# Kernel optimization log

Hardware: AMD Instinct MI355X
Metric: run time of the kernel (lower is better)

The kernel has to match this reference:

```python
import jax, jax.numpy as jnp
import numpy as np

B, T, D = 128, 32, 1024
ADA, INTER, RANK = 1024, 1024, 8
LN_EPS = 1e-5

def setup_inputs() -> dict:
    key = jax.random.key(0)
    ks = jax.random.split(key, 9)
    return {
        "x": jax.random.normal(ks[0], (B, T, D), dtype=jnp.float32),
        "ada_emb": jax.random.normal(ks[1], (B, ADA), dtype=jnp.float32),
        "base_layer": jax.random.normal(ks[2], (D, D), dtype=jnp.float32),  # torch.randn init
        "w1": jax.random.normal(ks[3], (ADA, INTER), dtype=jnp.float32) * 0.02,
        "b1": jnp.zeros((INTER,), dtype=jnp.float32),
        "w2": jax.random.normal(ks[4], (INTER, 2 * D * RANK), dtype=jnp.float32) * 0.02,
        "b2": jnp.zeros((2 * D * RANK,), dtype=jnp.float32),
        "ln_g": jnp.ones((ADA,), dtype=jnp.float32),
        "ln_b": jnp.zeros((ADA,), dtype=jnp.float32),
    }

def _layernorm(x, g, b):
    mu = jnp.mean(x, axis=-1, keepdims=True)
    var = jnp.var(x, axis=-1, keepdims=True)
    return (x - mu) * jax.lax.rsqrt(var + LN_EPS) * g + b

def reference(x, ada_emb, base_layer, w1, b1, w2, b2, ln_g, ln_b):
    b, t, d = x.shape
    # hypernetwork: cond -> per-sample LoRA factors
    ae = _layernorm(ada_emb, ln_g, ln_b)
    h = jax.nn.gelu(ae @ w1 + b1, approximate=False)  # nn.GELU is exact (erf)
    xw = h @ w2 + b2                                   # (B, 2*D*rank)
    x_a, x_b = jnp.split(xw, 2, axis=-1)
    x_a = x_a.reshape(b, d, RANK)
    x_b = x_b.reshape(b, d, RANK)
    # fused per-sample weight: base + x_a @ x_b^T  -> (B, D, D)
    layer = base_layer[None, :, :] + jnp.einsum('bdr,bkr->bdk', x_a, x_b)
    # apply shared per-sample weight to every token (equiv to repeat_interleave + bmm)
    out = jnp.einsum('btc,bco->bto', x, layer)
    return x + out  # residual=True
```

## Files before the change

kernel.cpp:

```cpp
#include <hip/hip_runtime.h>
#include <hip/hip_bf16.h>
#include <math.h>

#define BB    128
#define TT    32
#define DD    1024
#define NADA  1024
#define NINT  1024
#define NRANK 8
#define LNEPS 1e-5f
#define SPL2  8
#define XWN   (2 * DD * NRANK)

using bf16x8 = __attribute__((ext_vector_type(8))) short;
using f32x4  = __attribute__((ext_vector_type(4))) float;

__device__ __forceinline__ short f2bf(float f) {
    __hip_bfloat16 h = __float2bfloat16(f);
    return *reinterpret_cast<short*>(&h);
}

__device__ __forceinline__ void async16(const void* g, void* l) {
    __builtin_amdgcn_global_load_lds(
        (const __attribute__((address_space(1))) void*)g,
        (__attribute__((address_space(3))) void*)l, 16, 0, 0);
}

__device__ __forceinline__ void tcast_tile(
    const float* __restrict__ in, short* __restrict__ out, int K, int N,
    int bx, int by, bool addI, int tid, float (*t)[68])
{
    const int n0 = bx * 64, k0 = by * 64;
    #pragma unroll
    for (int it = 0; it < 4; ++it) {
        const int idx = it * 256 + tid;
        const int r = idx >> 4, c4 = (idx & 15) * 4;
        float4 v = *(const float4*)(in + (size_t)(k0 + r) * N + n0 + c4);
        t[r][c4 + 0] = v.x; t[r][c4 + 1] = v.y;
        t[r][c4 + 2] = v.z; t[r][c4 + 3] = v.w;
    }
    __syncthreads();
    #pragma unroll
    for (int it = 0; it < 4; ++it) {
        const int idx = it * 256 + tid;
        const int rn = idx >> 4, c4 = (idx & 15) * 4;
        float f0 = t[c4 + 0][rn], f1 = t[c4 + 1][rn];
        float f2 = t[c4 + 2][rn], f3 = t[c4 + 3][rn];
        if (addI) {
            const int n = n0 + rn;
            if (k0 + c4 + 0 == n) f0 += 1.f;
            if (k0 + c4 + 1 == n) f1 += 1.f;
            if (k0 + c4 + 2 == n) f2 += 1.f;
            if (k0 + c4 + 3 == n) f3 += 1.f;
        }
        short4 p;
        p.x = f2bf(f0); p.y = f2bf(f1); p.z = f2bf(f2); p.w = f2bf(f3);
        *(short4*)(out + (size_t)(n0 + rn) * K + k0 + c4) = p;
    }
}

__global__ __launch_bounds__(256) void prep_kernel(
    const float* __restrict__ x, const float* __restrict__ w1,
    const float* __restrict__ base, const float* __restrict__ ada,
    const float* __restrict__ lng, const float* __restrict__ lnb,
    short* __restrict__ x_bf, short* __restrict__ w1t,
    short* __restrict__ baset, short* __restrict__ ae_bf)
{
    __shared__ float t[64][68];
    const int bid = blockIdx.x, tid = threadIdx.x;

    if (bid < 2048) {
        const int i0 = bid * 512 + tid;
        float4 v0 = reinterpret_cast<const float4*>(x)[i0];
        float4 v1 = reinterpret_cast<const float4*>(x)[i0 + 256];
        short4 p0, p1;
        p0.x = f2bf(v0.x); p0.y = f2bf(v0.y); p0.z = f2bf(v0.z); p0.w = f2bf(v0.w);
        p1.x = f2bf(v1.x); p1.y = f2bf(v1.y); p1.z = f2bf(v1.z); p1.w = f2bf(v1.w);
        reinterpret_cast<short4*>(x_bf)[i0] = p0;
        reinterpret_cast<short4*>(x_bf)[i0 + 256] = p1;
    } else if (bid < 2304) {
        const int b = bid - 2048;
        tcast_tile(w1, w1t, NADA, NINT, b & 15, b >> 4, false, tid, t);
    } else if (bid < 2560) {
        const int b = bid - 2304;
        tcast_tile(base, baset, DD, DD, b & 15, b >> 4, true, tid, t);
    } else {
        const int b = bid - 2560;
        const float* row = ada + (size_t)b * NADA;
        float sum = 0.f, sumsq = 0.f;
        for (int i = tid; i < NADA; i += 256) {
            float v = row[i];
            sum += v; sumsq += v * v;
        }
        #pragma unroll
        for (int off = 32; off > 0; off >>= 1) {
            sum   += __shfl_down(sum, off);
            sumsq += __shfl_down(sumsq, off);
        }
        float* s1 = &t[0][0];
        float* s2 = &t[1][0];
        const int wid = tid >> 6, lane = tid & 63;
        if (lane == 0) { s1[wid] = sum; s2[wid] = sumsq; }
        __syncthreads();
        if (tid == 0) {
            float a = 0.f, c = 0.f;
            for (int i = 0; i < 4; ++i) { a += s1[i]; c += s2[i]; }
            s1[0] = a; s2[0] = c;
        }
        __syncthreads();
        const float mu  = s1[0] * (1.f / NADA);
        const float var = s2[0] * (1.f / NADA) - mu * mu;
        const float inv = rsqrtf(var + LNEPS);
        for (int i = tid; i < NADA; i += 256) {
            ae_bf[(size_t)b * NADA + i] = f2bf((row[i] - mu) * inv * lng[i] + lnb[i]);
        }
    }
}

__global__ __launch_bounds__(256, 2) void mgemm2(
    const short* __restrict__ A, const short* __restrict__ Bt,
    float* __restrict__ C, int kLen)
{
    constexpr int BM = 64, BN = 64;
    __shared__ __align__(16) short As[BM * 64];
    __shared__ __align__(16) short Bs[BN * 64];

    const int bm = blockIdx.y * BM;
    const int bn = blockIdx.x * BN;
    const int kStart = blockIdx.z * kLen;
    const int tid = threadIdx.x;
    const int wave = tid >> 6, lane = tid & 63;
    const int wm0 = (wave >> 1) * 32;
    const int wn0 = (wave & 1) * 32;
    const int quad = lane >> 4, r16 = lane & 15;

    f32x4 acc[2][2] = {};

    for (int kt = 0; kt < kLen; kt += 64) {
        const int k0 = kStart + kt;
        #pragma unroll
        for (int kk = 0; kk < 2; ++kk) {
            async16(A + (size_t)(bm + (tid >> 2)) * NADA + k0 + kk * 32 + (tid & 3) * 8,
                    &As[kk * 2048 + tid * 8]);
            async16(Bt + (size_t)(bn + (tid >> 2)) * NADA + k0 + kk * 32 + (tid & 3) * 8,
                    &Bs[kk * 2048 + tid * 8]);
        }
        __syncthreads();
        #pragma unroll
        for (int kk = 0; kk < 2; ++kk) {
            bf16x8 af[2], bfr[2];
            #pragma unroll
            for (int i = 0; i < 2; ++i)
                af[i] = *reinterpret_cast<const bf16x8*>(
                    &As[kk * 2048 + (wm0 + i * 16 + r16) * 32 + quad * 8]);
            #pragma unroll
            for (int j = 0; j < 2; ++j)
                bfr[j] = *reinterpret_cast<const bf16x8*>(
                    &Bs[kk * 2048 + (wn0 + j * 16 + r16) * 32 + quad * 8]);
            #pragma unroll
            for (int i = 0; i < 2; ++i)
                #pragma unroll
                for (int j = 0; j < 2; ++j)
                    acc[i][j] = __builtin_amdgcn_mfma_f32_16x16x32_bf16(
                        af[i], bfr[j], acc[i][j], 0, 0, 0);
        }
        __syncthreads();
    }

    #pragma unroll
    for (int i = 0; i < 2; ++i) {
        #pragma unroll
        for (int r = 0; r < 4; ++r) {
            const int m = bm + wm0 + i * 16 + quad * 4 + r;
            #pragma unroll
            for (int j = 0; j < 2; ++j) {
                const int n = bn + wn0 + j * 16 + r16;
                C[((size_t)blockIdx.z * BB + m) * NINT + n] = acc[i][j][r];
            }
        }
    }
}

__global__ __launch_bounds__(256) void combine_gelu(
    const float* __restrict__ part, const float* __restrict__ b1,
    short* __restrict__ h)
{
    const int i4 = (blockIdx.x * 256 + threadIdx.x) * 4;
    float4 s = *(const float4*)(b1 + (i4 & (NINT - 1)));
    #pragma unroll
    for (int z = 0; z < SPL2; ++z) {
        float4 p = *(const float4*)(part + (size_t)z * BB * NINT + i4);
        s.x += p.x; s.y += p.y; s.z += p.z; s.w += p.w;
    }
    s.x = 0.5f * s.x * (1.f + erff(s.x * 0.70710678118654752f));
    s.y = 0.5f * s.y * (1.f + erff(s.y * 0.70710678118654752f));
    s.z = 0.5f * s.z * (1.f + erff(s.z * 0.70710678118654752f));
    s.w = 0.5f * s.w * (1.f + erff(s.w * 0.70710678118654752f));
    short4 o;
    o.x = f2bf(s.x); o.y = f2bf(s.y); o.z = f2bf(s.z); o.w = f2bf(s.w);
    *(short4*)(h + i4) = o;
}

__global__ __launch_bounds__(256, 2) void gemm_w2(
    const short* __restrict__ A, const float* __restrict__ W,
    const float* __restrict__ b2,
    short* __restrict__ xat, float* __restrict__ xwb)
{
    constexpr int BN = 64;
    __shared__ __align__(16) short As[128 * 64];
    __shared__ __align__(16) float Bf[64 * BN];

    const int bn = blockIdx.x * BN;
    const int tid = threadIdx.x;
    const int wave = tid >> 6, lane = tid & 63;
    const int wm0 = (wave >> 1) * 64;
    const int wn0 = (wave & 1) * 32;
    const int quad = lane >> 4, r16 = lane & 15;

    f32x4 acc[4][2] = {};

    for (int kt = 0; kt < NINT; kt += 64) {
        #pragma unroll
        for (int kk = 0; kk < 2; ++kk) {
            #pragma unroll
            for (int s = 0; s < 2; ++s) {
                const int c = s * 256 + tid;
                async16(A + (size_t)(c >> 2) * NINT + kt + kk * 32 + (c & 3) * 8,
                        &As[kk * 4096 + c * 8]);
            }
            #pragma unroll
            for (int s = 0; s < 2; ++s) {
                const int c = s * 256 + tid;
                async16(W + (size_t)(kt + kk * 32 + (c >> 4)) * XWN + bn + (c & 15) * 4,
                        &Bf[kk * 2048 + c * 4]);
            }
        }
        __syncthreads();
        #pragma unroll
        for (int kk = 0; kk < 2; ++kk) {
            bf16x8 af[4], bfr[2];
            #pragma unroll
            for (int i = 0; i < 4; ++i)
                af[i] = *reinterpret_cast<const bf16x8*>(
                    &As[kk * 4096 + (wm0 + i * 16 + r16) * 32 + quad * 8]);
            #pragma unroll
            for (int j = 0; j < 2; ++j) {
                const int n = wn0 + j * 16 + r16;
                short tmp[8];
                #pragma unroll
                for (int t = 0; t < 8; ++t)
                    tmp[t] = f2bf(Bf[kk * 2048 + (quad * 8 + t) * BN + n]);
                bfr[j] = *reinterpret_cast<const bf16x8*>(tmp);
            }
            #pragma unroll
            for (int i = 0; i < 4; ++i)
                #pragma unroll
                for (int j = 0; j < 2; ++j)
                    acc[i][j] = __builtin_amdgcn_mfma_f32_16x16x32_bf16(
                        af[i], bfr[j], acc[i][j], 0, 0, 0);
        }
        __syncthreads();
    }

    const bool isA = (bn < DD * NRANK);
    #pragma unroll
    for (int i = 0; i < 4; ++i) {
        #pragma unroll
        for (int r = 0; r < 4; ++r) {
            const int m = wm0 + i * 16 + quad * 4 + r;
            #pragma unroll
            for (int j = 0; j < 2; ++j) {
                const int n = bn + wn0 + j * 16 + r16;
                const float v = acc[i][j][r] + b2[n];
                if (isA)
                    xat[(size_t)m * (NRANK * DD) + (n & 7) * DD + (n >> 3)] = f2bf(v);
                else
                    xwb[(size_t)m * (NRANK * DD) + (n - DD * NRANK)] = v;
            }
        }
    }
}

__global__ __launch_bounds__(256, 2) void fgemm(
    const short* __restrict__ A,
    const short* __restrict__ Bt,
    const short* __restrict__ xat,
    const float* __restrict__ xwb,
    float* __restrict__ C)
{
    __shared__ __align__(16) short As[128 * 64];
    __shared__ __align__(16) short Bs[64 * 64];
    __shared__ __align__(16) short xaS[32 * 64];
    __shared__ float tmS[128 * 8];
    __shared__ float xbS[4 * 64 * 8];

    const int bn = blockIdx.x * 64;
    const int bm = blockIdx.y * 128;
    const int b0 = bm >> 5;
    const int tid = threadIdx.x;
    const int wave = tid >> 6, lane = tid & 63;
    const int wm0 = (wave >> 1) * 64;
    const int wn0 = (wave & 1) * 32;
    const int quad = lane >> 4, r16 = lane & 15;
    const int w2s = (wave >> 1) * 2;

    {
        const int grp = tid >> 6, inner = tid & 63;
        const size_t off = (size_t)(b0 + grp) * (NRANK * DD) + (size_t)bn * 8 + inner * 8;
        float4 r0 = *(const float4*)(xwb + off);
        float4 r1 = *(const float4*)(xwb + off + 4);
        *(float4*)&xbS[grp * 512 + inner * 8]     = r0;
        *(float4*)&xbS[grp * 512 + inner * 8 + 4] = r1;
    }

    f32x4 acc[4][2] = {};
    f32x4 at[4] = {};

    for (int kt = 0; kt < DD; kt += 64) {
        #pragma unroll
        for (int kk = 0; kk < 2; ++kk) {
            #pragma unroll
            for (int s = 0; s < 2; ++s) {
                const int c = s * 256 + tid;
                async16(A + (size_t)(bm + (c >> 2)) * DD + kt + kk * 32 + (c & 3) * 8,
                        &As[kk * 4096 + c * 8]);
            }
            async16(Bt + (size_t)(bn + (tid >> 2)) * DD + kt + kk * 32 + (tid & 3) * 8,
                    &Bs[kk * 2048 + tid * 8]);
        }
        async16(xat + ((size_t)(b0 + (tid >> 6)) * 8 + ((tid >> 3) & 7)) * DD
                    + kt + (tid & 7) * 8,
                &xaS[(tid >> 3) * 64 + (tid & 7) * 8]);
        __syncthreads();
        #pragma unroll
        for (int kk = 0; kk < 2; ++kk) {
            bf16x8 af[4], bfr[2], bft[2];
            #pragma unroll
            for (int i = 0; i < 4; ++i)
                af[i] = *reinterpret_cast<const bf16x8*>(
                    &As[kk * 4096 + (wm0 + i * 16 + r16) * 32 + quad * 8]);
            #pragma unroll
            for (int j = 0; j < 2; ++j)
                bfr[j] = *reinterpret_cast<const bf16x8*>(
                    &Bs[kk * 2048 + (wn0 + j * 16 + r16) * 32 + quad * 8]);
            #pragma unroll
            for (int u = 0; u < 2; ++u)
                bft[u] = *reinterpret_cast<const bf16x8*>(
                    &xaS[((w2s + u) * 8 + (r16 & 7)) * 64 + kk * 32 + quad * 8]);
            #pragma unroll
            for (int i = 0; i < 4; ++i) {
                #pragma unroll
                for (int j = 0; j < 2; ++j)
                    acc[i][j] = __builtin_amdgcn_mfma_f32_16x16x32_bf16(
                        af[i], bfr[j], acc[i][j], 0, 0, 0);
                at[i] = __builtin_amdgcn_mfma_f32_16x16x32_bf16(
                    af[i], bft[i >> 1], at[i], 0, 0, 0);
            }
        }
        __syncthreads();
    }

    if (r16 < 8) {
        #pragma unroll
        for (int i = 0; i < 4; ++i)
            #pragma unroll
            for (int r = 0; r < 4; ++r)
                tmS[(wm0 + i * 16 + quad * 4 + r) * 8 + r16] = at[i][r];
    }
    __syncthreads();

    float xbr[2][8];
    #pragma unroll
    for (int i = 0; i < 4; ++i) {
        const int mlBase = wm0 + i * 16 + quad * 4;
        const int s = mlBase >> 5;
        #pragma unroll
        for (int j = 0; j < 2; ++j) {
            const int nl = wn0 + j * 16 + r16;
            #pragma unroll
            for (int rr = 0; rr < 8; ++rr)
                xbr[j][rr] = xbS[(s * 64 + nl) * 8 + rr];
        }
        #pragma unroll
        for (int r = 0; r < 4; ++r) {
            const int ml = mlBase + r;
            const int m = bm + ml;
            float t8[8];
            #pragma unroll
            for (int rr = 0; rr < 8; ++rr) t8[rr] = tmS[ml * 8 + rr];
            #pragma unroll
            for (int j = 0; j < 2; ++j) {
                const int n = bn + wn0 + j * 16 + r16;
                float v = acc[i][j][r];
                #pragma unroll
                for (int rr = 0; rr < 8; ++rr) v += t8[rr] * xbr[j][rr];
                C[(size_t)m * DD + n] = v;
            }
        }
    }
}

extern "C" void kernel_launch(void* const* d_in, const int* in_sizes, int n_in,
                              void* d_out, int out_size, void* d_ws, size_t ws_size,
                              hipStream_t stream)
{
    const float* x    = (const float*)d_in[0];
    const float* ada  = (const float*)d_in[1];
    const float* base = (const float*)d_in[2];
    const float* w1   = (const float*)d_in[3];
    const float* b1   = (const float*)d_in[4];
    const float* w2   = (const float*)d_in[5];
    const float* b2   = (const float*)d_in[6];
    const float* lng  = (const float*)d_in[7];
    const float* lnb  = (const float*)d_in[8];
    float* out = (float*)d_out;

    char* w = (char*)d_ws;
    short* x_bf  = (short*)w;  w += (size_t)8 << 20;
    short* w1t   = (short*)w;  w += (size_t)2 << 20;
    short* baset = (short*)w;  w += (size_t)2 << 20;
    short* ae_bf = (short*)w;  w += (size_t)256 << 10;
    short* h_bf  = (short*)w;  w += (size_t)256 << 10;
    short* xat   = (short*)w;  w += (size_t)2 << 20;
    float* xwb   = (float*)w;  w += (size_t)4 << 20;
    float* part  = (float*)w;

    prep_kernel<<<2688, 256, 0, stream>>>(
        x, w1, base, ada, lng, lnb, x_bf, w1t, baset, ae_bf);
    mgemm2<<<dim3(NINT / 64, BB / 64, SPL2), 256, 0, stream>>>(
        ae_bf, w1t, part, NADA / SPL2);
    combine_gelu<<<BB * NINT / 1024, 256, 0, stream>>>(part, b1, h_bf);
    gemm_w2<<<XWN / 64, 256, 0, stream>>>(h_bf, w2, b2, xat, xwb);
    fgemm<<<dim3(DD / 64, BB * TT / 128), 256, 0, stream>>>(
        x_bf, baset, xat, xwb, out);
}
```

Before: 181.0 us.

## Double-buffer fgemm LDS tiles, widen to 128x128 blocks, remap blocks per XCD

The final fused GEMM now uses 512-thread blocks covering 128x128 output tiles instead of 128x64, with double-buffered LDS stages so the next K tile's async loads overlap the current MFMA work. Blocks are remapped so each XCD handles a contiguous band of rows, which should improve L2 reuse of the A and base tiles. The change aims to cut load latency stalls and redundant global traffic. In exchange it uses more LDS per block and a 256-block grid, which may reduce occupancy.

```diff
diff --git a/kernel.cpp b/kernel.cpp
--- a/kernel.cpp
+++ b/kernel.cpp
@@ -281,72 +281,72 @@
     }
 }
 
-__global__ __launch_bounds__(256, 2) void fgemm(
+__global__ __launch_bounds__(512) void fgemm(
     const short* __restrict__ A,
     const short* __restrict__ Bt,
     const short* __restrict__ xat,
     const float* __restrict__ xwb,
     float* __restrict__ C)
 {
-    __shared__ __align__(16) short As[128 * 64];
-    __shared__ __align__(16) short Bs[64 * 64];
-    __shared__ __align__(16) short xaS[32 * 64];
+    __shared__ __align__(16) short As[2][128 * 64];
+    __shared__ __align__(16) short Bs[2][128 * 64];
+    __shared__ __align__(16) short xaS[2][32 * 64];
     __shared__ float tmS[128 * 8];
-    __shared__ float xbS[4 * 64 * 8];
-
-    const int bn = blockIdx.x * 64;
-    const int bm = blockIdx.y * 128;
-    const int b0 = bm >> 5;
+    __shared__ float xbS[4 * 128 * 8];
+
+    const int xcd = blockIdx.x & 7;
+    const int c   = blockIdx.x >> 3;
+    const int bm  = (xcd * 4 + (c >> 3)) * 128;
+    const int bn  = (c & 7) * 128;
+    const int b0  = bm >> 5;
     const int tid = threadIdx.x;
     const int wave = tid >> 6, lane = tid & 63;
-    const int wm0 = (wave >> 1) * 64;
-    const int wn0 = (wave & 1) * 32;
+    const int wm0 = (wave >> 2) * 64;
+    const int wn0 = (wave & 3) * 32;
     const int quad = lane >> 4, r16 = lane & 15;
-    const int w2s = (wave >> 1) * 2;
+    const int w2s = (wave >> 2) * 2;
 
     {
-        const int grp = tid >> 6, inner = tid & 63;
+        const int grp = tid >> 7, inner = tid & 127;
         const size_t off = (size_t)(b0 + grp) * (NRANK * DD) + (size_t)bn * 8 + inner * 8;
         float4 r0 = *(const float4*)(xwb + off);
         float4 r1 = *(const float4*)(xwb + off + 4);
-        *(float4*)&xbS[grp * 512 + inner * 8]     = r0;
-        *(float4*)&xbS[grp * 512 + inner * 8 + 4] = r1;
+        *(float4*)&xbS[grp * 1024 + inner * 8]     = r0;
+        *(float4*)&xbS[grp * 1024 + inner * 8 + 4] = r1;
     }
 
     f32x4 acc[4][2] = {};
     f32x4 at[4] = {};
 
-    for (int kt = 0; kt < DD; kt += 64) {
-        #pragma unroll
-        for (int kk = 0; kk < 2; ++kk) {
-            #pragma unroll
-            for (int s = 0; s < 2; ++s) {
-                const int c = s * 256 + tid;
-                async16(A + (size_t)(bm + (c >> 2)) * DD + kt + kk * 32 + (c & 3) * 8,
-                        &As[kk * 4096 + c * 8]);
-            }
-            async16(Bt + (size_t)(bn + (tid >> 2)) * DD + kt + kk * 32 + (tid & 3) * 8,
-                    &Bs[kk * 2048 + tid * 8]);
-        }
-        async16(xat + ((size_t)(b0 + (tid >> 6)) * 8 + ((tid >> 3) & 7)) * DD
-                    + kt + (tid & 7) * 8,
-                &xaS[(tid >> 3) * 64 + (tid & 7) * 8]);
-        __syncthreads();
+    auto stage = [&](int buf, int k0) {
+        #pragma unroll
+        for (int kk = 0; kk < 2; ++kk) {
+            async16(A + (size_t)(bm + (tid >> 2)) * DD + k0 + kk * 32 + (tid & 3) * 8,
+                    &As[buf][kk * 4096 + tid * 8]);
+            async16(Bt + (size_t)(bn + (tid >> 2)) * DD + k0 + kk * 32 + (tid & 3) * 8,
+                    &Bs[buf][kk * 4096 + tid * 8]);
+        }
+        if (tid < 256)
+            async16(xat + ((size_t)(b0 + (tid >> 6)) * 8 + ((tid >> 3) & 7)) * DD
+                        + k0 + (tid & 7) * 8,
+                    &xaS[buf][(tid >> 3) * 64 + (tid & 7) * 8]);
+    };
+    auto compute = [&](int buf) {
         #pragma unroll
         for (int kk = 0; kk < 2; ++kk) {
             bf16x8 af[4], bfr[2], bft[2];
             #pragma unroll
             for (int i = 0; i < 4; ++i)
                 af[i] = *reinterpret_cast<const bf16x8*>(
-                    &As[kk * 4096 + (wm0 + i * 16 + r16) * 32 + quad * 8]);
+                    &As[buf][kk * 4096 + (wm0 + i * 16 + r16) * 32 + quad * 8]);
             #pragma unroll
             for (int j = 0; j < 2; ++j)
                 bfr[j] = *reinterpret_cast<const bf16x8*>(
-                    &Bs[kk * 2048 + (wn0 + j * 16 + r16) * 32 + quad * 8]);
+                    &Bs[buf][kk * 4096 + (wn0 + j * 16 + r16) * 32 + quad * 8]);
             #pragma unroll
             for (int u = 0; u < 2; ++u)
                 bft[u] = *reinterpret_cast<const bf16x8*>(
-                    &xaS[((w2s + u) * 8 + (r16 & 7)) * 64 + kk * 32 + quad * 8]);
+                    &xaS[buf][((w2s + u) * 8 + (r16 & 7)) * 64 + kk * 32 + quad * 8]);
             #pragma unroll
             for (int i = 0; i < 4; ++i) {
                 #pragma unroll
@@ -357,10 +357,20 @@
                     af[i], bft[i >> 1], at[i], 0, 0, 0);
             }
         }
-        __syncthreads();
-    }
-
-    if (r16 < 8) {
+    };
+
+    stage(0, 0);
+    __syncthreads();
+    int cur = 0;
+    for (int kt = 64; kt < DD; kt += 64) {
+        stage(cur ^ 1, kt);
+        compute(cur);
+        __syncthreads();
+        cur ^= 1;
+    }
+    compute(cur);
+
+    if ((wave & 3) == 0 && r16 < 8) {
         #pragma unroll
         for (int i = 0; i < 4; ++i)
             #pragma unroll
@@ -379,7 +389,7 @@
             const int nl = wn0 + j * 16 + r16;
             #pragma unroll
             for (int rr = 0; rr < 8; ++rr)
-                xbr[j][rr] = xbS[(s * 64 + nl) * 8 + rr];
+                xbr[j][rr] = xbS[(s * 128 + nl) * 8 + rr];
         }
         #pragma unroll
         for (int r = 0; r < 4; ++r) {
@@ -431,6 +441,5 @@
         ae_bf, w1t, part, NADA / SPL2);
     combine_gelu<<<BB * NINT / 1024, 256, 0, stream>>>(part, b1, h_bf);
     gemm_w2<<<XWN / 64, 256, 0, stream>>>(h_bf, w2, b2, xat, xwb);
-    fgemm<<<dim3(DD / 64, BB * TT / 128), 256, 0, stream>>>(
-        x_bf, baset, xat, xwb, out);
-}
+    fgemm<<<256, 512, 0, stream>>>(x_bf, baset, xat, xwb, out);
+}
```

New measurement: 184.7 us. 1.02x slower.
